# Kernel optimization log

Hardware: AMD Instinct MI355X
Metric: run time of the kernel (lower is better)

The kernel has to match this reference:

```python
import jax, jax.numpy as jnp
import numpy as np

B, N = 16, 128
DN0, DE0, DH = 64, 16, 128  # input node dim, input edge dim, hidden dim


def _gnn2(A, x, e, w_msg, b_msg, w_node, b_node):
    """One GNN2 layer on dense batched graphs.
    A: [B,N,N] adjacency mask, x: [B,N,Dn], e: [B,N,N,De].
    Message/new-edge: relu(Linear([x_i, x_j, e_ij])) masked by A.
    New node: relu(Linear([x, sum_j msg_ij])).
    The concat-Linear is decomposed into three matmuls to avoid
    materializing the [B,N,N,2Dn+De] concat tensor.
    """
    Dn = x.shape[-1]
    Wi, Wj, We = w_msg[:Dn], w_msg[Dn:2 * Dn], w_msg[2 * Dn:]
    xi = x @ Wi                                   # [B,N,Do]
    xj = x @ Wj                                   # [B,N,Do]
    msg = jax.nn.relu(xi[:, :, None, :] + xj[:, None, :, :] + e @ We + b_msg)
    msg = msg * A[..., None]                      # mask non-edges -> new edge_attr [B,N,N,Do]
    agg = msg.sum(axis=2)                         # scatter-sum over neighbors j -> [B,N,Do]
    Wx, Wa = w_node[:Dn], w_node[Dn:]
    x_new = jax.nn.relu(x @ Wx + agg @ Wa + b_node)
    return x_new, msg


def setup_inputs() -> dict:
    key = jax.random.key(0)
    ks = iter(jax.random.split(key, 32))
    s = 0.05
    inp = {
        "edge_index": jax.random.randint(next(ks), (B, N, N), 0, 2, dtype=jnp.int32),
        "x": jax.random.normal(next(ks), (B, N, DN0), dtype=jnp.float32),
        "edge_attr": jax.random.normal(next(ks), (B, N, N, DE0), dtype=jnp.float32),
    }
    def w(shape):
        return s * jax.random.normal(next(ks), shape, dtype=jnp.float32)
    # layer 0: node_in=64, edge_in=16 -> 128
    inp["w_msg_0"], inp["b_msg_0"] = w((2 * DN0 + DE0, DH)), w((DH,))
    inp["w_node_0"], inp["b_node_0"] = w((DN0 + DH, DH)), w((DH,))
    # layers 1,2: 128 -> 128
    for l in (1, 2):
        inp[f"w_msg_{l}"], inp[f"b_msg_{l}"] = w((2 * DH + DH, DH)), w((DH,))
        inp[f"w_node_{l}"], inp[f"b_node_{l}"] = w((DH + DH, DH)), w((DH,))
    # head mlp: 128 -> 128 -> 128 -> 1
    inp["w_h1"], inp["b_h1"] = w((DH, DH)), w((DH,))
    inp["w_h2"], inp["b_h2"] = w((DH, DH)), w((DH,))
    inp["w_h3"], inp["b_h3"] = w((DH, 1)), w((1,))
    return inp


def reference(edge_index, x, edge_attr,
              w_msg_0, b_msg_0, w_node_0, b_node_0,
              w_msg_1, b_msg_1, w_node_1, b_node_1,
              w_msg_2, b_msg_2, w_node_2, b_node_2,
              w_h1, b_h1, w_h2, b_h2, w_h3, b_h3):
    A = edge_index.astype(jnp.float32)
    x = x.astype(jnp.float32)
    # layer 0
    x, e = _gnn2(A, x, edge_attr, w_msg_0, b_msg_0, w_node_0, b_node_0)
    # middle layer with 0.5 residual blend
    x_, e_ = _gnn2(A, x, e, w_msg_1, b_msg_1, w_node_1, b_node_1)
    x = 0.5 * (x + x_)
    e = 0.5 * (e + e_)
    # last layer
    x, e = _gnn2(A, x, e, w_msg_2, b_msg_2, w_node_2, b_node_2)
    # edge_mean readout + MLP head
    h = e.mean(axis=(1, 2))                       # [B, DH]
    h = jax.nn.relu(h @ w_h1 + b_h1)
    h = jax.nn.relu(h @ w_h2 + b_h2)
    out = h @ w_h3 + b_h3                         # [B, 1]
    return out.squeeze(-1)                        # [B]
```

## Files before the change

### kernel.cpp

```cpp
#include <hip/hip_runtime.h>

constexpr int B = 16, N = 128, D = 128, DN0 = 64, DE0 = 16;

typedef _Float16 half8 __attribute__((ext_vector_type(8)));
typedef _Float16 half4 __attribute__((ext_vector_type(4)));
typedef float floatx4 __attribute__((ext_vector_type(4)));
typedef float floatx16 __attribute__((ext_vector_type(16)));

__device__ __forceinline__ void gld16(const _Float16* g, _Float16* l) {
  __builtin_amdgcn_global_load_lds(
      (const __attribute__((address_space(1))) void*)g,
      (__attribute__((address_space(3))) void*)l, 16, 0, 0);
}

__global__ __launch_bounds__(256) void k_pre(
    const float* __restrict__ x, const float* __restrict__ wm0,
    const float* __restrict__ bm0, const float* __restrict__ wm1,
    const float* __restrict__ wm2,
    float* __restrict__ xi0, float* __restrict__ xj0,
    _Float16* __restrict__ weT1, _Float16* __restrict__ weT2) {
  const int bid = blockIdx.x;
  const int t = threadIdx.x;
  if (bid < B * N) {
    const int row = bid;
    const int half = t >> 7, c = t & 127;
    __shared__ float xr[DN0];
    if (t < DN0) xr[t] = x[(size_t)row * DN0 + t];
    __syncthreads();
    float a = half ? 0.f : bm0[c];
    const float* wb = wm0 + half * DN0 * D;
    #pragma unroll 32
    for (int k = 0; k < DN0; ++k) a = fmaf(xr[k], wb[k * D + c], a);
    (half ? xj0 : xi0)[(size_t)row * D + c] = a;
  } else {
    const int g = (bid - B * N) * 256 + t;
    const int layer = g >> 14;
    const int rem = g & 16383;
    const int c = rem >> 7, k = rem & 127;
    const float* src = layer ? wm2 : wm1;
    _Float16* dst = layer ? weT2 : weT1;
    dst[rem] = (_Float16)src[(2 * D + k) * D + c];
  }
}

__global__ __launch_bounds__(256) void k_edge0(
    const int* __restrict__ ei, const float* __restrict__ eattr,
    const float* __restrict__ wm0,
    const float* __restrict__ xi0, const float* __restrict__ xj0,
    _Float16* __restrict__ msg0, float* __restrict__ agg0) {
  const int row = blockIdx.x;
  const int b = row >> 7;
  const int t = threadIdx.x;
  const int c8 = (t & 15) * 8, jr = t >> 4;

  __shared__ float eb[N * 20];
  __shared__ float w_t[DE0][D];
  __shared__ float amask[N];
  __shared__ float xi_r[D];
  float* hp = eb;

  const float4* esrc = (const float4*)(eattr + (size_t)row * N * DE0);
  const float4* wsrc = (const float4*)(wm0 + 2 * DN0 * D);
  #pragma unroll
  for (int u = 0; u < 2; ++u) {
    const int idx4 = u * 256 + t;
    const int j = idx4 >> 2;
    const int k4 = (idx4 & 3) * 4;
    *(float4*)&eb[j * 20 + k4] = esrc[idx4];
    ((float4*)&w_t[0][0])[idx4] = wsrc[idx4];
  }
  if (t < N) {
    amask[t] = (float)ei[(size_t)row * N + t];
    xi_r[t] = xi0[(size_t)row * D + t];
  }
  __syncthreads();

  float acc[8][8] = {};
  #pragma unroll 4
  for (int k = 0; k < DE0; ++k) {
    float av[8];
    #pragma unroll
    for (int p = 0; p < 8; ++p) av[p] = eb[(16 * p + jr) * 20 + k];
    const floatx4 wv0 = *(const floatx4*)&w_t[k][c8];
    const floatx4 wv1 = *(const floatx4*)&w_t[k][c8 + 4];
    #pragma unroll
    for (int p = 0; p < 8; ++p)
      #pragma unroll
      for (int q = 0; q < 4; ++q) {
        acc[p][q]     = fmaf(av[p], wv0[q], acc[p][q]);
        acc[p][4 + q] = fmaf(av[p], wv1[q], acc[p][4 + q]);
      }
  }

  float acc8[8] = {};
  const float* xjb = xj0 + (size_t)b * N * D;
  _Float16* mrow = msg0 + (size_t)row * N * D;
  const floatx4 xiv0 = *(const floatx4*)&xi_r[c8];
  const floatx4 xiv1 = *(const floatx4*)&xi_r[c8 + 4];
  #pragma unroll
  for (int p = 0; p < 8; ++p) {
    const int j = 16 * p + jr;
    const float am = amask[j];
    const floatx4 xjv0 = *(const floatx4*)&xjb[j * D + c8];
    const floatx4 xjv1 = *(const floatx4*)&xjb[j * D + c8 + 4];
    half8 hv;
    #pragma unroll
    for (int q = 0; q < 4; ++q) {
      float v0 = fmaxf(xiv0[q] + xjv0[q] + acc[p][q], 0.f) * am;
      float v1 = fmaxf(xiv1[q] + xjv1[q] + acc[p][4 + q], 0.f) * am;
      hv[q] = (_Float16)v0;
      hv[4 + q] = (_Float16)v1;
      acc8[q] += v0;
      acc8[4 + q] += v1;
    }
    if (am != 0.f)
      *(half8*)&mrow[j * D + (((t & 15) ^ jr) << 3)] = hv;
  }

  __syncthreads();
  #pragma unroll
  for (int q = 0; q < 8; ++q) hp[(jr * 16 + (t & 15)) * 8 + q] = acc8[q];
  __syncthreads();
  if (t < D) {
    float s = 0.f;
    #pragma unroll
    for (int g = 0; g < 16; ++g) s += hp[(g * 16 + (t >> 3)) * 8 + (t & 7)];
    agg0[(size_t)row * D + t] = s;
  }
}

__global__ __launch_bounds__(256) void k_node1(
    const float* __restrict__ x0, const float* __restrict__ agg0,
    const float* __restrict__ wn0, const float* __restrict__ bn0,
    const float* __restrict__ wm1, const float* __restrict__ bm1,
    float* __restrict__ x1, float* __restrict__ xi1, float* __restrict__ xj1) {
  const int r0 = blockIdx.x * 8;
  const int t = threadIdx.x;
  const int c = t & 127, rh = t >> 7;
  __shared__ float sIn[8][DN0];
  __shared__ float sAg[8][D];
  __shared__ float sX1[8][D];
  ((float2*)&sIn[0][0])[t] = ((const float2*)(x0 + (size_t)r0 * DN0))[t];
  ((float4*)&sAg[0][0])[t] = ((const float4*)(agg0 + (size_t)r0 * D))[t];
  __syncthreads();

  float acc[4];
  #pragma unroll
  for (int r = 0; r < 4; ++r) acc[r] = bn0[c];
  #pragma unroll 4
  for (int k4 = 0; k4 < DN0; k4 += 4) {
    const float* wb = wn0 + k4 * D + c;
    const float w0 = wb[0], w1 = wb[D], w2 = wb[2 * D], w3 = wb[3 * D];
    #pragma unroll
    for (int r = 0; r < 4; ++r) {
      const float4 xv = *(const float4*)&sIn[rh * 4 + r][k4];
      acc[r] = fmaf(xv.x, w0, acc[r]);
      acc[r] = fmaf(xv.y, w1, acc[r]);
      acc[r] = fmaf(xv.z, w2, acc[r]);
      acc[r] = fmaf(xv.w, w3, acc[r]);
    }
  }
  #pragma unroll 4
  for (int k4 = 0; k4 < D; k4 += 4) {
    const float* wb = wn0 + (DN0 + k4) * D + c;
    const float w0 = wb[0], w1 = wb[D], w2 = wb[2 * D], w3 = wb[3 * D];
    #pragma unroll
    for (int r = 0; r < 4; ++r) {
      const float4 xv = *(const float4*)&sAg[rh * 4 + r][k4];
      acc[r] = fmaf(xv.x, w0, acc[r]);
      acc[r] = fmaf(xv.y, w1, acc[r]);
      acc[r] = fmaf(xv.z, w2, acc[r]);
      acc[r] = fmaf(xv.w, w3, acc[r]);
    }
  }
  #pragma unroll
  for (int r = 0; r < 4; ++r) {
    const float v = fmaxf(acc[r], 0.f);
    sX1[rh * 4 + r][c] = v;
    x1[(size_t)(r0 + rh * 4 + r) * D + c] = v;
  }
  __syncthreads();

  float a[8];
  #pragma unroll
  for (int r = 0; r < 8; ++r) a[r] = rh ? 0.f : bm1[c];
  const float* wh = wm1 + (size_t)rh * D * D;
  #pragma unroll 2
  for (int k4 = 0; k4 < D; k4 += 4) {
    const float* wb = wh + k4 * D + c;
    const float w0 = wb[0], w1 = wb[D], w2 = wb[2 * D], w3 = wb[3 * D];
    #pragma unroll
    for (int r = 0; r < 8; ++r) {
      const float4 xv = *(const float4*)&sX1[r][k4];
      a[r] = fmaf(xv.x, w0, a[r]);
      a[r] = fmaf(xv.y, w1, a[r]);
      a[r] = fmaf(xv.z, w2, a[r]);
      a[r] = fmaf(xv.w, w3, a[r]);
    }
  }
  float* dst = rh ? xj1 : xi1;
  #pragma unroll
  for (int r = 0; r < 8; ++r) dst[(size_t)(r0 + r) * D + c] = a[r];
}

__global__ __launch_bounds__(256, 2) void k_mid(
    const int* __restrict__ ei, const _Float16* __restrict__ weT1,
    const _Float16* __restrict__ weT2,
    const float* __restrict__ xi, const float* __restrict__ xj,
    _Float16* __restrict__ em,
    float* __restrict__ agg1) {
  const int row = blockIdx.x;
  const int b = row >> 7;
  const int t = threadIdx.x;
  const int w = t >> 6;
  const int lane = t & 63;
  const int l31 = lane & 31;
  const int l15 = lane & 15;
  const int hl = lane >> 5;

  __shared__ _Float16 sE[N * D];
  __shared__ float sMask[N];

  const _Float16* gsrc = em + (size_t)row * N * D;
  #pragma unroll
  for (int u = 0; u < 8; ++u) {
    const int seg = (u * 4 + w) * 512;
    gld16(gsrc + seg + lane * 8, &sE[seg]);
  }

  half8 a1[8];
  #pragma unroll
  for (int ks = 0; ks < 8; ++ks)
    a1[ks] = *(const half8*)(weT1 + (32 * w + l31) * D + 16 * ks + 8 * hl);

  floatx4 xiv[4];
  #pragma unroll
  for (int g = 0; g < 4; ++g)
    xiv[g] = *(const floatx4*)&xi[(size_t)row * D + 32 * w + 8 * g + 4 * hl];
  if (t < N) sMask[t] = (float)ei[(size_t)row * N + t];

  __syncthreads();

  float am[4];
  #pragma unroll
  for (int jt = 0; jt < 4; ++jt) am[jt] = sMask[32 * jt + l31];

  const floatx16 vzero = {0.f,0.f,0.f,0.f,0.f,0.f,0.f,0.f,
                          0.f,0.f,0.f,0.f,0.f,0.f,0.f,0.f};
  floatx16 acc[4];
  #pragma unroll
  for (int jt = 0; jt < 4; ++jt) acc[jt] = vzero;
  #pragma unroll
  for (int ks = 0; ks < 8; ++ks)
    #pragma unroll
    for (int jt = 0; jt < 4; ++jt) {
      const half8 bv = *(const half8*)
          &sE[(32 * jt + l31) * D + (((2 * ks + hl) ^ l15) << 3)];
      acc[jt] = __builtin_amdgcn_mfma_f32_32x32x16_f16(a1[ks], bv, acc[jt], 0, 0, 0);
    }

  __syncthreads();

  const float* xjb = xj + (size_t)b * N * D;
  floatx4 hacc[4];
  #pragma unroll
  for (int g = 0; g < 4; ++g) hacc[g] = (floatx4){0.f, 0.f, 0.f, 0.f};
  #pragma unroll
  for (int jt = 0; jt < 4; ++jt) {
    const int j = 32 * jt + l31;
    #pragma unroll
    for (int g = 0; g < 4; ++g) {
      const int cofs = 32 * w + 8 * g + 4 * hl;
      const int hidx = j * D + (((4 * w + g) ^ l15) << 3) + 4 * hl;
      const floatx4 xjv = *(const floatx4*)&xjb[j * D + cofs];
      const half4 m0 = *(const half4*)&sE[hidx];
      half4 mid;
      floatx4 m1;
      #pragma unroll
      for (int r = 0; r < 4; ++r) {
        const float v = xiv[g][r] + xjv[r] + acc[jt][4 * g + r];
        m1[r] = fmaxf(v, 0.f) * am[jt];
        mid[r] = (_Float16)(0.5f * ((float)m0[r] + m1[r]));
      }
      *(half4*)&sE[hidx] = mid;
      hacc[g] += m1;
    }
  }

  #pragma unroll
  for (int m = 1; m < 32; m <<= 1)
    #pragma unroll
    for (int g = 0; g < 4; ++g)
      #pragma unroll
      for (int r = 0; r < 4; ++r)
        hacc[g][r] += __shfl_xor(hacc[g][r], m, 64);
  if (l31 == 0) {
    #pragma unroll
    for (int g = 0; g < 4; ++g)
      *(floatx4*)&agg1[(size_t)row * D + 32 * w + 8 * g + 4 * hl] = hacc[g];
  }

  half8 a2[8];
  #pragma unroll
  for (int ks = 0; ks < 8; ++ks)
    a2[ks] = *(const half8*)(weT2 + (32 * w + l31) * D + 16 * ks + 8 * hl);

  __syncthreads();

  #pragma unroll
  for (int jt = 0; jt < 4; ++jt) acc[jt] = vzero;
  #pragma unroll
  for (int ks = 0; ks < 8; ++ks)
    #pragma unroll
    for (int jt = 0; jt < 4; ++jt) {
      const half8 bv = *(const half8*)
          &sE[(32 * jt + l31) * D + (((2 * ks + hl) ^ l15) << 3)];
      acc[jt] = __builtin_amdgcn_mfma_f32_32x32x16_f16(a2[ks], bv, acc[jt], 0, 0, 0);
    }

  __syncthreads();

  #pragma unroll
  for (int jt = 0; jt < 4; ++jt) {
    const int j = 32 * jt + l31;
    #pragma unroll
    for (int g = 0; g < 4; ++g) {
      const int hidx = j * D + (((4 * w + g) ^ l15) << 3) + 4 * hl;
      half4 tv;
      #pragma unroll
      for (int r = 0; r < 4; ++r) tv[r] = (_Float16)acc[jt][4 * g + r];
      *(half4*)&sE[hidx] = tv;
    }
  }

  __syncthreads();

  uint4* gdst = (uint4*)(em + (size_t)row * N * D);
  const uint4* ls = (const uint4*)sE;
  #pragma unroll
  for (int u = 0; u < 8; ++u) {
    const int idx4 = u * 256 + t;
    const int j = u * 16 + (t >> 4);
    if (sMask[j] != 0.f) gdst[idx4] = ls[idx4];
  }
}

__global__ __launch_bounds__(256) void k_node2(
    const float* __restrict__ x1, const float* __restrict__ agg1,
    const float* __restrict__ wn1, const float* __restrict__ bn1,
    const float* __restrict__ wm2, const float* __restrict__ bm2,
    float* __restrict__ xi2, float* __restrict__ xj2) {
  const int r0 = blockIdx.x * 8;
  const int t = threadIdx.x;
  const int c = t & 127, rh = t >> 7;
  __shared__ float sIn[8][D];
  __shared__ float sAg[8][D];
  __shared__ float sXm[8][D];
  ((float4*)&sIn[0][0])[t] = ((const float4*)(x1 + (size_t)r0 * D))[t];
  ((float4*)&sAg[0][0])[t] = ((const float4*)(agg1 + (size_t)r0 * D))[t];
  __syncthreads();

  float acc[4];
  #pragma unroll
  for (int r = 0; r < 4; ++r) acc[r] = bn1[c];
  #pragma unroll 4
  for (int k4 = 0; k4 < D; k4 += 4) {
    const float* wb = wn1 + k4 * D + c;
    const float w0 = wb[0], w1 = wb[D], w2 = wb[2 * D], w3 = wb[3 * D];
    #pragma unroll
    for (int r = 0; r < 4; ++r) {
      const float4 xv = *(const float4*)&sIn[rh * 4 + r][k4];
      acc[r] = fmaf(xv.x, w0, acc[r]);
      acc[r] = fmaf(xv.y, w1, acc[r]);
      acc[r] = fmaf(xv.z, w2, acc[r]);
      acc[r] = fmaf(xv.w, w3, acc[r]);
    }
  }
  #pragma unroll 4
  for (int k4 = 0; k4 < D; k4 += 4) {
    const float* wb = wn1 + (D + k4) * D + c;
    const float w0 = wb[0], w1 = wb[D], w2 = wb[2 * D], w3 = wb[3 * D];
    #pragma unroll
    for (int r = 0; r < 4; ++r) {
      const float4 xv = *(const float4*)&sAg[rh * 4 + r][k4];
      acc[r] = fmaf(xv.x, w0, acc[r]);
      acc[r] = fmaf(xv.y, w1, acc[r]);
      acc[r] = fmaf(xv.z, w2, acc[r]);
      acc[r] = fmaf(xv.w, w3, acc[r]);
    }
  }
  #pragma unroll
  for (int r = 0; r < 4; ++r) {
    const float v = 0.5f * (sIn[rh * 4 + r][c] + fmaxf(acc[r], 0.f));
    sXm[rh * 4 + r][c] = v;
  }
  __syncthreads();

  float a[8];
  #pragma unroll
  for (int r = 0; r < 8; ++r) a[r] = rh ? 0.f : bm2[c];
  const float* wh = wm2 + (size_t)rh * D * D;
  #pragma unroll 2
  for (int k4 = 0; k4 < D; k4 += 4) {
    const float* wb = wh + k4 * D + c;
    const float w0 = wb[0], w1 = wb[D], w2 = wb[2 * D], w3 = wb[3 * D];
    #pragma unroll
    for (int r = 0; r < 8; ++r) {
      const float4 xv = *(const float4*)&sXm[r][k4];
      a[r] = fmaf(xv.x, w0, a[r]);
      a[r] = fmaf(xv.y, w1, a[r]);
      a[r] = fmaf(xv.z, w2, a[r]);
      a[r] = fmaf(xv.w, w3, a[r]);
    }
  }
  float* dst = rh ? xj2 : xi2;
  #pragma unroll
  for (int r = 0; r < 8; ++r) dst[(size_t)(r0 + r) * D + c] = a[r];
}

__global__ __launch_bounds__(256) void k_fin(
    const int* __restrict__ ei, const _Float16* __restrict__ t2,
    const float* __restrict__ xi, const float* __restrict__ xj,
    float* __restrict__ rowsum) {
  const int row = blockIdx.x;
  const int b = row >> 7;
  const int t = threadIdx.x;
  const int c8 = (t & 15) * 8, jr = t >> 4;

  __shared__ float sMask[N];
  __shared__ float hp[16][16][8];
  if (t < N) sMask[t] = (float)ei[(size_t)row * N + t];
  float xiv[8];
  *(floatx4*)&xiv[0] = *(const floatx4*)&xi[row * D + c8];
  *(floatx4*)&xiv[4] = *(const floatx4*)&xi[row * D + c8 + 4];
  __syncthreads();

  const _Float16* src = t2 + (size_t)row * N * D;
  const float* xjb = xj + (size_t)b * N * D;
  float acc8[8] = {};
  #pragma unroll
  for (int u = 0; u < 8; ++u) {
    const int j = u * 16 + jr;
    if (sMask[j] != 0.f) {
      const half8 tv = *(const half8*)(src + j * D + (((t & 15) ^ jr) << 3));
      const floatx4 xj0 = *(const floatx4*)&xjb[j * D + c8];
      const floatx4 xj1 = *(const floatx4*)&xjb[j * D + c8 + 4];
      #pragma unroll
      for (int r = 0; r < 4; ++r) {
        acc8[r]     += fmaxf(xiv[r] + xj0[r] + (float)tv[r], 0.f);
        acc8[4 + r] += fmaxf(xiv[4 + r] + xj1[r] + (float)tv[4 + r], 0.f);
      }
    }
  }
  #pragma unroll
  for (int k = 0; k < 8; ++k) hp[jr][t & 15][k] = acc8[k];
  __syncthreads();
  if (t < D) {
    float s = 0.f;
    #pragma unroll
    for (int g = 0; g < 16; ++g) s += hp[g][t >> 3][t & 7];
    rowsum[row * D + t] = s;
  }
}

__global__ __launch_bounds__(128) void k_head(
    const float* __restrict__ rowsum,
    const float* __restrict__ w1, const float* __restrict__ b1,
    const float* __restrict__ w2, const float* __restrict__ b2,
    const float* __restrict__ w3, const float* __restrict__ b3,
    float* __restrict__ out) {
  const int b = blockIdx.x;
  const int c = threadIdx.x;
  __shared__ float hr[D], h1r[D], h2r[D];
  const float* rs = rowsum + (size_t)b * N * D;
  float s = 0.f;
  for (int i = 0; i < N; ++i) s += rs[i * D + c];
  hr[c] = s * (1.f / (N * N));
  __syncthreads();
  float a = b1[c];
  #pragma unroll 8
  for (int k = 0; k < D; ++k) a = fmaf(hr[k], w1[k * D + c], a);
  h1r[c] = fmaxf(a, 0.f);
  __syncthreads();
  a = b2[c];
  #pragma unroll 8
  for (int k = 0; k < D; ++k) a = fmaf(h1r[k], w2[k * D + c], a);
  h2r[c] = fmaxf(a, 0.f);
  __syncthreads();
  hr[c] = h2r[c] * w3[c];
  __syncthreads();
  if (c == 0) {
    float s2 = b3[0];
    for (int k = 0; k < D; ++k) s2 += hr[k];
    out[b] = s2;
  }
}

extern "C" void kernel_launch(void* const* d_in, const int* in_sizes, int n_in,
                              void* d_out, int out_size, void* d_ws, size_t ws_size,
                              hipStream_t stream) {
  const int*   ei  = (const int*)d_in[0];
  const float* x0  = (const float*)d_in[1];
  const float* ea  = (const float*)d_in[2];
  const float* wm0 = (const float*)d_in[3];
  const float* bm0 = (const float*)d_in[4];
  const float* wn0 = (const float*)d_in[5];
  const float* bn0 = (const float*)d_in[6];
  const float* wm1 = (const float*)d_in[7];
  const float* bm1 = (const float*)d_in[8];
  const float* wn1 = (const float*)d_in[9];
  const float* bn1 = (const float*)d_in[10];
  const float* wm2 = (const float*)d_in[11];
  const float* bm2 = (const float*)d_in[12];
  const float* wh1 = (const float*)d_in[15];
  const float* bh1 = (const float*)d_in[16];
  const float* wh2 = (const float*)d_in[17];
  const float* bh2 = (const float*)d_in[18];
  const float* wh3 = (const float*)d_in[19];
  const float* bh3 = (const float*)d_in[20];
  float* out = (float*)d_out;

  _Float16* msg0h = (_Float16*)d_ws;
  _Float16* weT1  = msg0h + (size_t)B * N * N * D;
  _Float16* weT2  = weT1 + D * D;
  float* f = (float*)(weT2 + D * D);
  size_t off = 0;
  const size_t R = (size_t)B * N * D;
  float* xi0  = f + off; off += R;
  float* xj0  = f + off; off += R;
  float* x1   = f + off; off += R;
  float* xi1  = f + off; off += R;
  float* xj1  = f + off; off += R;
  float* xi2  = f + off; off += R;
  float* xj2  = f + off; off += R;
  float* rsum = f + off; off += R;

  float* aggS = rsum;

  const int rows = B * N;
  k_pre  <<<rows + 128, 256, 0, stream>>>(x0, wm0, bm0, wm1, wm2,
                                          xi0, xj0, weT1, weT2);
  k_edge0<<<rows, 256, 0, stream>>>(ei, ea, wm0, xi0, xj0, msg0h, aggS);
  k_node1<<<rows / 8, 256, 0, stream>>>(x0, aggS, wn0, bn0, wm1, bm1,
                                        x1, xi1, xj1);
  k_mid  <<<rows, 256, 0, stream>>>(ei, weT1, weT2, xi1, xj1, msg0h, aggS);
  k_node2<<<rows / 8, 256, 0, stream>>>(x1, aggS, wn1, bn1, wm2, bm2,
                                        xi2, xj2);
  k_fin  <<<rows, 256, 0, stream>>>(ei, msg0h, xi2, xj2, rsum);
  k_head <<<B,    128, 0, stream>>>(rsum, wh1, bh1, wh2, bh2, wh3, bh3, out);
}
```

Before: 222.4 us.

## Split k_mid over neighbor halves and halve node-kernel row tiles

k_mid now runs two blocks per row, each handling 64 of the 128 neighbors. Each block writes a partial aggregate to its own buffer, and k_node2 sums the two buffers. This halves shared memory per block, raises the occupancy hint from 2 to 4 blocks per CU, and doubles the grid so more work runs in flight. k_node1 and k_node2 now process 4 rows per block instead of 8, which gives twice as many blocks but less weight reuse per block. The cost is that xi and the weight fragments are loaded twice per row, plus an extra partial-aggregate buffer that reuses the xi0 workspace.

```diff
diff --git a/kernel.cpp b/kernel.cpp
--- a/kernel.cpp
+++ b/kernel.cpp
@@ -134,26 +134,26 @@
     const float* __restrict__ wn0, const float* __restrict__ bn0,
     const float* __restrict__ wm1, const float* __restrict__ bm1,
     float* __restrict__ x1, float* __restrict__ xi1, float* __restrict__ xj1) {
-  const int r0 = blockIdx.x * 8;
+  const int r0 = blockIdx.x * 4;
   const int t = threadIdx.x;
   const int c = t & 127, rh = t >> 7;
-  __shared__ float sIn[8][DN0];
-  __shared__ float sAg[8][D];
-  __shared__ float sX1[8][D];
-  ((float2*)&sIn[0][0])[t] = ((const float2*)(x0 + (size_t)r0 * DN0))[t];
-  ((float4*)&sAg[0][0])[t] = ((const float4*)(agg0 + (size_t)r0 * D))[t];
-  __syncthreads();
-
-  float acc[4];
-  #pragma unroll
-  for (int r = 0; r < 4; ++r) acc[r] = bn0[c];
+  __shared__ float sIn[4][DN0];
+  __shared__ float sAg[4][D];
+  __shared__ float sX1[4][D];
+  ((float*)sIn)[t] = x0[(size_t)r0 * DN0 + t];
+  ((float2*)sAg)[t] = ((const float2*)(agg0 + (size_t)r0 * D))[t];
+  __syncthreads();
+
+  float acc[2];
+  #pragma unroll
+  for (int r = 0; r < 2; ++r) acc[r] = bn0[c];
   #pragma unroll 4
   for (int k4 = 0; k4 < DN0; k4 += 4) {
     const float* wb = wn0 + k4 * D + c;
     const float w0 = wb[0], w1 = wb[D], w2 = wb[2 * D], w3 = wb[3 * D];
     #pragma unroll
-    for (int r = 0; r < 4; ++r) {
-      const float4 xv = *(const float4*)&sIn[rh * 4 + r][k4];
+    for (int r = 0; r < 2; ++r) {
+      const float4 xv = *(const float4*)&sIn[rh * 2 + r][k4];
       acc[r] = fmaf(xv.x, w0, acc[r]);
       acc[r] = fmaf(xv.y, w1, acc[r]);
       acc[r] = fmaf(xv.z, w2, acc[r]);
@@ -165,8 +165,8 @@
     const float* wb = wn0 + (DN0 + k4) * D + c;
     const float w0 = wb[0], w1 = wb[D], w2 = wb[2 * D], w3 = wb[3 * D];
     #pragma unroll
-    for (int r = 0; r < 4; ++r) {
-      const float4 xv = *(const float4*)&sAg[rh * 4 + r][k4];
+    for (int r = 0; r < 2; ++r) {
+      const float4 xv = *(const float4*)&sAg[rh * 2 + r][k4];
       acc[r] = fmaf(xv.x, w0, acc[r]);
       acc[r] = fmaf(xv.y, w1, acc[r]);
       acc[r] = fmaf(xv.z, w2, acc[r]);
@@ -174,23 +174,23 @@
     }
   }
   #pragma unroll
-  for (int r = 0; r < 4; ++r) {
+  for (int r = 0; r < 2; ++r) {
     const float v = fmaxf(acc[r], 0.f);
-    sX1[rh * 4 + r][c] = v;
-    x1[(size_t)(r0 + rh * 4 + r) * D + c] = v;
-  }
-  __syncthreads();
-
-  float a[8];
-  #pragma unroll
-  for (int r = 0; r < 8; ++r) a[r] = rh ? 0.f : bm1[c];
+    sX1[rh * 2 + r][c] = v;
+    x1[(size_t)(r0 + rh * 2 + r) * D + c] = v;
+  }
+  __syncthreads();
+
+  float a[4];
+  #pragma unroll
+  for (int r = 0; r < 4; ++r) a[r] = rh ? 0.f : bm1[c];
   const float* wh = wm1 + (size_t)rh * D * D;
-  #pragma unroll 2
+  #pragma unroll 4
   for (int k4 = 0; k4 < D; k4 += 4) {
     const float* wb = wh + k4 * D + c;
     const float w0 = wb[0], w1 = wb[D], w2 = wb[2 * D], w3 = wb[3 * D];
     #pragma unroll
-    for (int r = 0; r < 8; ++r) {
+    for (int r = 0; r < 4; ++r) {
       const float4 xv = *(const float4*)&sX1[r][k4];
       a[r] = fmaf(xv.x, w0, a[r]);
       a[r] = fmaf(xv.y, w1, a[r]);
@@ -200,16 +200,17 @@
   }
   float* dst = rh ? xj1 : xi1;
   #pragma unroll
-  for (int r = 0; r < 8; ++r) dst[(size_t)(r0 + r) * D + c] = a[r];
-}
-
-__global__ __launch_bounds__(256, 2) void k_mid(
+  for (int r = 0; r < 4; ++r) dst[(size_t)(r0 + r) * D + c] = a[r];
+}
+
+__global__ __launch_bounds__(256, 4) void k_mid(
     const int* __restrict__ ei, const _Float16* __restrict__ weT1,
     const _Float16* __restrict__ weT2,
     const float* __restrict__ xi, const float* __restrict__ xj,
     _Float16* __restrict__ em,
-    float* __restrict__ agg1) {
-  const int row = blockIdx.x;
+    float* __restrict__ agg1p0, float* __restrict__ agg1p1) {
+  const int row = blockIdx.x >> 1;
+  const int jh = blockIdx.x & 1;
   const int b = row >> 7;
   const int t = threadIdx.x;
   const int w = t >> 6;
@@ -218,12 +219,12 @@
   const int l15 = lane & 15;
   const int hl = lane >> 5;
 
-  __shared__ _Float16 sE[N * D];
-  __shared__ float sMask[N];
-
-  const _Float16* gsrc = em + (size_t)row * N * D;
-  #pragma unroll
-  for (int u = 0; u < 8; ++u) {
+  __shared__ _Float16 sE[64 * D];
+  __shared__ float sMask[64];
+
+  const _Float16* gsrc = em + (size_t)row * N * D + (size_t)jh * 64 * D;
+  #pragma unroll
+  for (int u = 0; u < 4; ++u) {
     const int seg = (u * 4 + w) * 512;
     gld16(gsrc + seg + lane * 8, &sE[seg]);
   }
@@ -237,23 +238,23 @@
   #pragma unroll
   for (int g = 0; g < 4; ++g)
     xiv[g] = *(const floatx4*)&xi[(size_t)row * D + 32 * w + 8 * g + 4 * hl];
-  if (t < N) sMask[t] = (float)ei[(size_t)row * N + t];
-
-  __syncthreads();
-
-  float am[4];
-  #pragma unroll
-  for (int jt = 0; jt < 4; ++jt) am[jt] = sMask[32 * jt + l31];
+  if (t < 64) sMask[t] = (float)ei[(size_t)row * N + 64 * jh + t];
+
+  __syncthreads();
+
+  float am[2];
+  #pragma unroll
+  for (int jt = 0; jt < 2; ++jt) am[jt] = sMask[32 * jt + l31];
 
   const floatx16 vzero = {0.f,0.f,0.f,0.f,0.f,0.f,0.f,0.f,
                           0.f,0.f,0.f,0.f,0.f,0.f,0.f,0.f};
-  floatx16 acc[4];
-  #pragma unroll
-  for (int jt = 0; jt < 4; ++jt) acc[jt] = vzero;
+  floatx16 acc[2];
+  #pragma unroll
+  for (int jt = 0; jt < 2; ++jt) acc[jt] = vzero;
   #pragma unroll
   for (int ks = 0; ks < 8; ++ks)
     #pragma unroll
-    for (int jt = 0; jt < 4; ++jt) {
+    for (int jt = 0; jt < 2; ++jt) {
       const half8 bv = *(const half8*)
           &sE[(32 * jt + l31) * D + (((2 * ks + hl) ^ l15) << 3)];
       acc[jt] = __builtin_amdgcn_mfma_f32_32x32x16_f16(a1[ks], bv, acc[jt], 0, 0, 0);
@@ -266,13 +267,14 @@
   #pragma unroll
   for (int g = 0; g < 4; ++g) hacc[g] = (floatx4){0.f, 0.f, 0.f, 0.f};
   #pragma unroll
-  for (int jt = 0; jt < 4; ++jt) {
-    const int j = 32 * jt + l31;
+  for (int jt = 0; jt < 2; ++jt) {
+    const int jl = 32 * jt + l31;
+    const int jg = 64 * jh + jl;
     #pragma unroll
     for (int g = 0; g < 4; ++g) {
       const int cofs = 32 * w + 8 * g + 4 * hl;
-      const int hidx = j * D + (((4 * w + g) ^ l15) << 3) + 4 * hl;
-      const floatx4 xjv = *(const floatx4*)&xjb[j * D + cofs];
+      const int hidx = jl * D + (((4 * w + g) ^ l15) << 3) + 4 * hl;
+      const floatx4 xjv = *(const floatx4*)&xjb[jg * D + cofs];
       const half4 m0 = *(const half4*)&sE[hidx];
       half4 mid;
       floatx4 m1;
@@ -295,9 +297,10 @@
       for (int r = 0; r < 4; ++r)
         hacc[g][r] += __shfl_xor(hacc[g][r], m, 64);
   if (l31 == 0) {
+    float* aggp = jh ? agg1p1 : agg1p0;
     #pragma unroll
     for (int g = 0; g < 4; ++g)
-      *(floatx4*)&agg1[(size_t)row * D + 32 * w + 8 * g + 4 * hl] = hacc[g];
+      *(floatx4*)&aggp[(size_t)row * D + 32 * w + 8 * g + 4 * hl] = hacc[g];
   }
 
   half8 a2[8];
@@ -308,11 +311,11 @@
   __syncthreads();
 
   #pragma unroll
-  for (int jt = 0; jt < 4; ++jt) acc[jt] = vzero;
+  for (int jt = 0; jt < 2; ++jt) acc[jt] = vzero;
   #pragma unroll
   for (int ks = 0; ks < 8; ++ks)
     #pragma unroll
-    for (int jt = 0; jt < 4; ++jt) {
+    for (int jt = 0; jt < 2; ++jt) {
       const half8 bv = *(const half8*)
           &sE[(32 * jt + l31) * D + (((2 * ks + hl) ^ l15) << 3)];
       acc[jt] = __builtin_amdgcn_mfma_f32_32x32x16_f16(a2[ks], bv, acc[jt], 0, 0, 0);
@@ -321,11 +324,11 @@
   __syncthreads();
 
   #pragma unroll
-  for (int jt = 0; jt < 4; ++jt) {
-    const int j = 32 * jt + l31;
+  for (int jt = 0; jt < 2; ++jt) {
+    const int jl = 32 * jt + l31;
     #pragma unroll
     for (int g = 0; g < 4; ++g) {
-      const int hidx = j * D + (((4 * w + g) ^ l15) << 3) + 4 * hl;
+      const int hidx = jl * D + (((4 * w + g) ^ l15) << 3) + 4 * hl;
       half4 tv;
       #pragma unroll
       for (int r = 0; r < 4; ++r) tv[r] = (_Float16)acc[jt][4 * g + r];
@@ -335,41 +338,46 @@
 
   __syncthreads();
 
-  uint4* gdst = (uint4*)(em + (size_t)row * N * D);
+  uint4* gdst = (uint4*)(em + (size_t)row * N * D + (size_t)jh * 64 * D);
   const uint4* ls = (const uint4*)sE;
   #pragma unroll
-  for (int u = 0; u < 8; ++u) {
+  for (int u = 0; u < 4; ++u) {
     const int idx4 = u * 256 + t;
-    const int j = u * 16 + (t >> 4);
-    if (sMask[j] != 0.f) gdst[idx4] = ls[idx4];
+    const int jl = u * 16 + (t >> 4);
+    if (sMask[jl] != 0.f) gdst[idx4] = ls[idx4];
   }
 }
 
 __global__ __launch_bounds__(256) void k_node2(
-    const float* __restrict__ x1, const float* __restrict__ agg1,
+    const float* __restrict__ x1,
+    const float* __restrict__ agg1p0, const float* __restrict__ agg1p1,
     const float* __restrict__ wn1, const float* __restrict__ bn1,
     const float* __restrict__ wm2, const float* __restrict__ bm2,
     float* __restrict__ xi2, float* __restrict__ xj2) {
-  const int r0 = blockIdx.x * 8;
+  const int r0 = blockIdx.x * 4;
   const int t = threadIdx.x;
   const int c = t & 127, rh = t >> 7;
-  __shared__ float sIn[8][D];
-  __shared__ float sAg[8][D];
-  __shared__ float sXm[8][D];
-  ((float4*)&sIn[0][0])[t] = ((const float4*)(x1 + (size_t)r0 * D))[t];
-  ((float4*)&sAg[0][0])[t] = ((const float4*)(agg1 + (size_t)r0 * D))[t];
-  __syncthreads();
-
-  float acc[4];
-  #pragma unroll
-  for (int r = 0; r < 4; ++r) acc[r] = bn1[c];
+  __shared__ float sIn[4][D];
+  __shared__ float sAg[4][D];
+  __shared__ float sXm[4][D];
+  ((float2*)sIn)[t] = ((const float2*)(x1 + (size_t)r0 * D))[t];
+  {
+    const float2 g0 = ((const float2*)(agg1p0 + (size_t)r0 * D))[t];
+    const float2 g1 = ((const float2*)(agg1p1 + (size_t)r0 * D))[t];
+    ((float2*)sAg)[t] = make_float2(g0.x + g1.x, g0.y + g1.y);
+  }
+  __syncthreads();
+
+  float acc[2];
+  #pragma unroll
+  for (int r = 0; r < 2; ++r) acc[r] = bn1[c];
   #pragma unroll 4
   for (int k4 = 0; k4 < D; k4 += 4) {
     const float* wb = wn1 + k4 * D + c;
     const float w0 = wb[0], w1 = wb[D], w2 = wb[2 * D], w3 = wb[3 * D];
     #pragma unroll
-    for (int r = 0; r < 4; ++r) {
-      const float4 xv = *(const float4*)&sIn[rh * 4 + r][k4];
+    for (int r = 0; r < 2; ++r) {
+      const float4 xv = *(const float4*)&sIn[rh * 2 + r][k4];
       acc[r] = fmaf(xv.x, w0, acc[r]);
       acc[r] = fmaf(xv.y, w1, acc[r]);
       acc[r] = fmaf(xv.z, w2, acc[r]);
@@ -381,8 +389,8 @@
     const float* wb = wn1 + (D + k4) * D + c;
     const float w0 = wb[0], w1 = wb[D], w2 = wb[2 * D], w3 = wb[3 * D];
     #pragma unroll
-    for (int r = 0; r < 4; ++r) {
-      const float4 xv = *(const float4*)&sAg[rh * 4 + r][k4];
+    for (int r = 0; r < 2; ++r) {
+      const float4 xv = *(const float4*)&sAg[rh * 2 + r][k4];
       acc[r] = fmaf(xv.x, w0, acc[r]);
       acc[r] = fmaf(xv.y, w1, acc[r]);
       acc[r] = fmaf(xv.z, w2, acc[r]);
@@ -390,22 +398,22 @@
     }
   }
   #pragma unroll
-  for (int r = 0; r < 4; ++r) {
-    const float v = 0.5f * (sIn[rh * 4 + r][c] + fmaxf(acc[r], 0.f));
-    sXm[rh * 4 + r][c] = v;
-  }
-  __syncthreads();
-
-  float a[8];
-  #pragma unroll
-  for (int r = 0; r < 8; ++r) a[r] = rh ? 0.f : bm2[c];
+  for (int r = 0; r < 2; ++r) {
+    const float v = 0.5f * (sIn[rh * 2 + r][c] + fmaxf(acc[r], 0.f));
+    sXm[rh * 2 + r][c] = v;
+  }
+  __syncthreads();
+
+  float a[4];
+  #pragma unroll
+  for (int r = 0; r < 4; ++r) a[r] = rh ? 0.f : bm2[c];
   const float* wh = wm2 + (size_t)rh * D * D;
-  #pragma unroll 2
+  #pragma unroll 4
   for (int k4 = 0; k4 < D; k4 += 4) {
     const float* wb = wh + k4 * D + c;
     const float w0 = wb[0], w1 = wb[D], w2 = wb[2 * D], w3 = wb[3 * D];
     #pragma unroll
-    for (int r = 0; r < 8; ++r) {
+    for (int r = 0; r < 4; ++r) {
       const float4 xv = *(const float4*)&sXm[r][k4];
       a[r] = fmaf(xv.x, w0, a[r]);
       a[r] = fmaf(xv.y, w1, a[r]);
@@ -415,7 +423,7 @@
   }
   float* dst = rh ? xj2 : xi2;
   #pragma unroll
-  for (int r = 0; r < 8; ++r) dst[(size_t)(r0 + r) * D + c] = a[r];
+  for (int r = 0; r < 4; ++r) dst[(size_t)(r0 + r) * D + c] = a[r];
 }
 
 __global__ __launch_bounds__(256) void k_fin(
@@ -536,15 +544,18 @@
   float* rsum = f + off; off += R;
 
   float* aggS = rsum;
+  float* a1p0 = rsum;
+  float* a1p1 = xi0;
 
   const int rows = B * N;
   k_pre  <<<rows + 128, 256, 0, stream>>>(x0, wm0, bm0, wm1, wm2,
                                           xi0, xj0, weT1, weT2);
   k_edge0<<<rows, 256, 0, stream>>>(ei, ea, wm0, xi0, xj0, msg0h, aggS);
-  k_node1<<<rows / 8, 256, 0, stream>>>(x0, aggS, wn0, bn0, wm1, bm1,
+  k_node1<<<rows / 4, 256, 0, stream>>>(x0, aggS, wn0, bn0, wm1, bm1,
                                         x1, xi1, xj1);
-  k_mid  <<<rows, 256, 0, stream>>>(ei, weT1, weT2, xi1, xj1, msg0h, aggS);
-  k_node2<<<rows / 8, 256, 0, stream>>>(x1, aggS, wn1, bn1, wm2, bm2,
+  k_mid  <<<rows * 2, 256, 0, stream>>>(ei, weT1, weT2, xi1, xj1, msg0h,
+                                        a1p0, a1p1);
+  k_node2<<<rows / 4, 256, 0, stream>>>(x1, a1p0, a1p1, wn1, bn1, wm2, bm2,
                                         xi2, xj2);
   k_fin  <<<rows, 256, 0, stream>>>(ei, msg0h, xi2, xj2, rsum);
   k_head <<<B,    128, 0, stream>>>(rsum, wh1, bh1, wh2, bh2, wh3, bh3, out);
```

After: 231.0 us. 1.04x slower.
